# Optimization experiments

Measured on AMD Instinct MI355X. Metric: run time of the kernel, lower is better.

## Reference

```python
import jax, jax.numpy as jnp
import numpy as np

B, CH1, CH2, HID, T, E = 64, 3, 4, 16, 16384, 512

def setup_inputs() -> dict:
    key = jax.random.key(0)
    ks = jax.random.split(key, 12)
    s_t = 1.0 / np.sqrt(T)   # fan_in = input_dim for q/k/v projections
    s_e = 1.0 / np.sqrt(E)   # fan_in = embed_dim for out_proj
    return {
        "x":  jax.random.normal(ks[0], (B, 7, T), jnp.float32),
        "W1": jax.random.normal(ks[1], (HID, CH1), jnp.float32) / np.sqrt(CH1),
        "W2": jax.random.normal(ks[2], (HID, CH2), jnp.float32) / np.sqrt(CH2),
        "Wq": jax.random.normal(ks[3], (E, T), jnp.float32) * s_t,
        "bq": jnp.zeros((E,), jnp.float32),
        "Wk": jax.random.normal(ks[4], (E, T), jnp.float32) * s_t,
        "bk": jnp.zeros((E,), jnp.float32),
        "Wv": jax.random.normal(ks[5], (E, T), jnp.float32) * s_t,
        "bv": jnp.zeros((E,), jnp.float32),
        "Wo": jax.random.normal(ks[6], (T, E), jnp.float32) * s_e,
        "bo": jnp.zeros((T,), jnp.float32),
        "W3": jax.random.normal(ks[7], (CH1, HID), jnp.float32) / np.sqrt(HID),
    }

def reference(x, W1, W2, Wq, bq, Wk, bk, Wv, bv, Wo, bo, W3):
    p = x[:, :CH1]            # [B,3,T]  narrow(1,0,ch_1)
    c = x[:, 3:3 + CH2]       # [B,4,T]  narrow(1,3,ch_2)
    q = jnp.einsum('oc,bct->bot', W1, p)   # fc_1: [B,16,T]
    cc = jnp.einsum('oc,bct->bot', W2, c)  # fc_2: [B,16,T]
    # CrossAttention: Linears act on last dim (T -> E)
    Q = jnp.einsum('bct,et->bce', q, Wq) + bq    # [B,16,E]
    K = jnp.einsum('bct,et->bce', cc, Wk) + bk   # [B,16,E]
    V = jnp.einsum('bct,et->bce', cc, Wv) + bv   # [B,16,E]
    scale = 1.0 / np.sqrt(HID)                   # nch = 16 query channels
    attn_w = jax.nn.softmax(jnp.einsum('bce,bcf->bef', Q, K) * scale, axis=-1)  # [B,E,E]
    attn = jnp.einsum('bef,bcf->bce', attn_w, V)  # [B,16,E]
    out = jnp.einsum('bce,te->bct', attn, Wo) + bo  # out_proj: [B,16,T]
    y = jnp.einsum('oc,bct->bot', W3, out)          # fc_3: [B,3,T]
    return p + y
```

## Files before the change

kernel.cpp:

```cpp
#include <hip/hip_runtime.h>

#define BB 64
#define TT 16384
#define EE 512

typedef _Float16 half8 __attribute__((ext_vector_type(8)));
typedef float floatx4 __attribute__((ext_vector_type(4)));

static __device__ __forceinline__ half8 cvt_half8(float4 a, float4 b) {
  half8 h;
  h[0] = (_Float16)a.x; h[1] = (_Float16)a.y; h[2] = (_Float16)a.z; h[3] = (_Float16)a.w;
  h[4] = (_Float16)b.x; h[5] = (_Float16)b.y; h[6] = (_Float16)b.z; h[7] = (_Float16)b.w;
  return h;
}

static __device__ __forceinline__ void gload_lds16(const void* g, void* l) {
  __builtin_amdgcn_global_load_lds(
      (const __attribute__((address_space(1))) void*)g,
      (__attribute__((address_space(3))) void*)l, 16, 0, 0);
}

__global__ __launch_bounds__(256) void zero_ws(float4* __restrict__ p) {
  p[blockIdx.x * 256 + threadIdx.x] = (float4){0.f, 0.f, 0.f, 0.f};
}

__global__ __launch_bounds__(256) void proj_gemm(
    const float* __restrict__ x, const float* __restrict__ Wq,
    const float* __restrict__ Wk, const float* __restrict__ Wv,
    float* __restrict__ Xq, float* __restrict__ Xkv)
{
  __shared__ float Abuf[3][64 * 32];
  __shared__ float Bbuf[3][64 * 32];
  const int t = threadIdx.x;
  const int wave = t >> 6, lane = t & 63;
  const int quad = lane >> 4, l16 = lane & 15;
  const int wr = wave >> 1, wc = wave & 1;

  const int orig = blockIdx.x;
  const int logical = (orig & 7) * 352 + (orig >> 3);
  const int chunk = logical / 88;
  const int tile  = logical - chunk * 88;
  const int k0 = chunk << 9;

  int mtile, ntile, cpb, chan_base, ldout;
  const float* Wsrc;
  float* outC;
  if (tile < 24) {
    mtile = tile >> 3; ntile = tile & 7;
    cpb = 3; chan_base = 0; ldout = 512;
    Wsrc = Wq + (size_t)(ntile * 64) * TT;
    outC = Xq;
  } else {
    const int t2 = tile - 24;
    mtile = t2 >> 4; ntile = t2 & 15;
    cpb = 4; chan_base = 3; ldout = 1024;
    Wsrc = (ntile < 8) ? (Wk + (size_t)(ntile * 64) * TT)
                       : (Wv + (size_t)((ntile - 8) * 64) * TT);
    outC = Xkv;
  }

  const float* aSrc[2];
  const float* bSrc[2];
#pragma unroll
  for (int r = 0; r < 2; ++r) {
    const int i = (r * 4 + wave) * 64 + lane;
    const int row = i >> 3, u = i & 7;
    const int m = mtile * 64 + row;
    const int bidx = (cpb == 3) ? ((m * 21846) >> 16) : (m >> 2);
    const int j = m - bidx * cpb;
    const int swu = (u ^ (row & 7)) << 2;
    aSrc[r] = x + (size_t)(bidx * 7 + chan_base + j) * TT + k0 + swu;
    bSrc[r] = Wsrc + (size_t)row * TT + k0 + swu;
  }

  floatx4 acc[2][2];
#pragma unroll
  for (int rt = 0; rt < 2; ++rt)
#pragma unroll
    for (int ct = 0; ct < 2; ++ct)
      acc[rt][ct] = (floatx4){0.f, 0.f, 0.f, 0.f};

  const int sw = l16 & 7;

  auto stage = [&](int kt_, int buf_) {
    const int ko = kt_ * 32;
#pragma unroll
    for (int r = 0; r < 2; ++r) {
      gload_lds16(aSrc[r] + ko, &Abuf[buf_][(r * 4 + wave) * 256]);
      gload_lds16(bSrc[r] + ko, &Bbuf[buf_][(r * 4 + wave) * 256]);
    }
  };
  auto compute = [&](int buf_) {
    half8 hb[2], ha[2];
#pragma unroll
    for (int ct = 0; ct < 2; ++ct) {
      const int brow = wc * 32 + ct * 16 + l16;
      float4 b0 = *(const float4*)&Bbuf[buf_][brow * 32 + ((((quad << 1) | 0) ^ sw) << 2)];
      float4 b1 = *(const float4*)&Bbuf[buf_][brow * 32 + ((((quad << 1) | 1) ^ sw) << 2)];
      hb[ct] = cvt_half8(b0, b1);
    }
#pragma unroll
    for (int rt = 0; rt < 2; ++rt) {
      const int arow = wr * 32 + rt * 16 + l16;
      float4 a0 = *(const float4*)&Abuf[buf_][arow * 32 + ((((quad << 1) | 0) ^ sw) << 2)];
      float4 a1 = *(const float4*)&Abuf[buf_][arow * 32 + ((((quad << 1) | 1) ^ sw) << 2)];
      ha[rt] = cvt_half8(a0, a1);
    }
    __builtin_amdgcn_s_setprio(1);
#pragma unroll
    for (int rt = 0; rt < 2; ++rt)
#pragma unroll
      for (int ct = 0; ct < 2; ++ct)
        acc[rt][ct] = __builtin_amdgcn_mfma_f32_16x16x32_f16(ha[rt], hb[ct], acc[rt][ct], 0, 0, 0);
    __builtin_amdgcn_s_setprio(0);
  };

  stage(0, 0);
  stage(1, 1);
  asm volatile("s_waitcnt vmcnt(4)" ::: "memory");
  __builtin_amdgcn_s_barrier();
  __builtin_amdgcn_sched_barrier(0);

  int cur = 0;
#pragma unroll
  for (int kt = 0; kt < 14; ++kt) {
    const int nx2 = (cur + 2 >= 3) ? cur - 1 : cur + 2;
    stage(kt + 2, nx2);
    compute(cur);
    asm volatile("s_waitcnt vmcnt(4)" ::: "memory");
    __builtin_amdgcn_s_barrier();
    __builtin_amdgcn_sched_barrier(0);
    cur = (cur + 1 >= 3) ? 0 : cur + 1;
  }
  compute(cur);
  asm volatile("s_waitcnt vmcnt(0)" ::: "memory");
  __builtin_amdgcn_s_barrier();
  __builtin_amdgcn_sched_barrier(0);
  compute((cur + 1 >= 3) ? 0 : cur + 1);

#pragma unroll
  for (int rt = 0; rt < 2; ++rt) {
#pragma unroll
    for (int ct = 0; ct < 2; ++ct) {
      const int gr = mtile * 64 + wr * 32 + rt * 16 + quad * 4;
      const int gc = ntile * 64 + wc * 32 + ct * 16 + l16;
#pragma unroll
      for (int rg = 0; rg < 4; ++rg)
        atomicAdd(&outC[(size_t)(gr + rg) * ldout + gc], acc[rt][ct][rg]);
    }
  }
}

__global__ __launch_bounds__(256) void attn_mid(
    const float* __restrict__ Xq, const float* __restrict__ Xkv,
    const float* __restrict__ W1, const float* __restrict__ W2,
    const float* __restrict__ W3,
    const float* __restrict__ bq, const float* __restrict__ bk,
    const float* __restrict__ bv, _Float16* __restrict__ U)
{
  __shared__ float Ks[16][512];
  __shared__ float VW[3][512];
  __shared__ float Qs[16][64];
  __shared__ float Xs[4][512];
  __shared__ float W1s[48], W2s[64], W3s[48], W32s[12], w3sum[3];
  const int t = threadIdx.x;
  const int b = blockIdx.y;
  const int e0 = blockIdx.x * 64;

  if (t < 48) W1s[t] = W1[t];
  if (t >= 64 && t < 128) W2s[t - 64] = W2[t - 64];
  if (t >= 128 && t < 176) W3s[t - 128] = W3[t - 128];
  __syncthreads();
  if (t < 12) {
    const int o = t >> 2, jj = t & 3;
    float s = 0.f;
    for (int c = 0; c < 16; ++c) s += W3s[o * 16 + c] * W2s[c * 4 + jj];
    W32s[t] = s;
  }
  if (t >= 16 && t < 19) {
    const int o = t - 16;
    float s = 0.f;
    for (int c = 0; c < 16; ++c) s += W3s[o * 16 + c];
    w3sum[o] = s;
  }
  for (int i = t; i < 2048; i += 256) {
    const int jj = i >> 9, f = i & 511;
    Xs[jj][f] = Xkv[(size_t)(b * 4 + jj) * 1024 + f];
  }
  __syncthreads();
  for (int i = t; i < 8192; i += 256) {
    const int c = i >> 9, f = i & 511;
    float s = bk[f];
#pragma unroll
    for (int jj = 0; jj < 4; ++jj) s += W2s[c * 4 + jj] * Xs[jj][f];
    Ks[c][f] = s;
  }
  __syncthreads();
  for (int i = t; i < 2048; i += 256) {
    const int jj = i >> 9, f = i & 511;
    Xs[jj][f] = Xkv[(size_t)(b * 4 + jj) * 1024 + 512 + f];
  }
  __syncthreads();
  for (int i = t; i < 1536; i += 256) {
    const int o = i >> 9, f = i & 511;
    float s = w3sum[o] * bv[f];
#pragma unroll
    for (int jj = 0; jj < 4; ++jj) s += W32s[o * 4 + jj] * Xs[jj][f];
    VW[o][f] = s;
  }
  for (int i = t; i < 1024; i += 256) {
    const int c = i >> 6, el = i & 63;
    float s = bq[e0 + el];
#pragma unroll
    for (int jj = 0; jj < 3; ++jj)
      s += W1s[c * 3 + jj] * Xq[(size_t)(b * 3 + jj) * 512 + e0 + el];
    Qs[c][el] = s;
  }
  __syncthreads();

  const int wave = t >> 6, lane = t & 63;
  float vwr[3][8];
#pragma unroll
  for (int o = 0; o < 3; ++o) {
    float4 va = *(const float4*)&VW[o][lane * 8];
    float4 vb = *(const float4*)&VW[o][lane * 8 + 4];
    vwr[o][0] = va.x; vwr[o][1] = va.y; vwr[o][2] = va.z; vwr[o][3] = va.w;
    vwr[o][4] = vb.x; vwr[o][5] = vb.y; vwr[o][6] = vb.z; vwr[o][7] = vb.w;
  }

  for (int g = 0; g < 4; ++g) {
    const int el0 = wave * 16 + g * 4;
    float s[4][8];
#pragma unroll
    for (int e = 0; e < 4; ++e)
#pragma unroll
      for (int i = 0; i < 8; ++i) s[e][i] = 0.f;
#pragma unroll
    for (int c = 0; c < 16; ++c) {
      float4 k0 = *(const float4*)&Ks[c][lane * 8];
      float4 k1 = *(const float4*)&Ks[c][lane * 8 + 4];
      float4 qv = *(const float4*)&Qs[c][el0];
      float qa[4] = {qv.x, qv.y, qv.z, qv.w};
#pragma unroll
      for (int e = 0; e < 4; ++e) {
        const float q = qa[e];
        s[e][0] += q * k0.x; s[e][1] += q * k0.y; s[e][2] += q * k0.z; s[e][3] += q * k0.w;
        s[e][4] += q * k1.x; s[e][5] += q * k1.y; s[e][6] += q * k1.z; s[e][7] += q * k1.w;
      }
    }
#pragma unroll
    for (int e = 0; e < 4; ++e) {
      float mx = s[e][0];
#pragma unroll
      for (int i = 1; i < 8; ++i) mx = fmaxf(mx, s[e][i]);
#pragma unroll
      for (int off = 32; off; off >>= 1) mx = fmaxf(mx, __shfl_xor(mx, off));
      float p[8], sum = 0.f;
#pragma unroll
      for (int i = 0; i < 8; ++i) { p[i] = __expf(0.25f * (s[e][i] - mx)); sum += p[i]; }
      float u0 = 0.f, u1 = 0.f, u2 = 0.f;
#pragma unroll
      for (int i = 0; i < 8; ++i) {
        u0 += p[i] * vwr[0][i];
        u1 += p[i] * vwr[1][i];
        u2 += p[i] * vwr[2][i];
      }
#pragma unroll
      for (int off = 32; off; off >>= 1) {
        sum += __shfl_xor(sum, off);
        u0  += __shfl_xor(u0, off);
        u1  += __shfl_xor(u1, off);
        u2  += __shfl_xor(u2, off);
      }
      if (lane == 0) {
        const float inv = 1.0f / sum;
        const size_t base = (size_t)b * 3 * 512 + (e0 + el0 + e);
        U[base]        = (_Float16)(u0 * inv);
        U[base + 512]  = (_Float16)(u1 * inv);
        U[base + 1024] = (_Float16)(u2 * inv);
      }
    }
  }
}

__global__ __launch_bounds__(256) void out_gemm(
    const _Float16* __restrict__ U, const float* __restrict__ Wo,
    const float* __restrict__ x, const float* __restrict__ bo,
    const float* __restrict__ W3, float* __restrict__ outY)
{
  __shared__ _Float16 Au[3][64 * 32];
  __shared__ float    Bw[3][64 * 32];
  const int t = threadIdx.x;
  const int wave = t >> 6, lane = t & 63;
  const int quad = lane >> 4, l16 = lane & 15;
  const int mtile = blockIdx.y, ntile = blockIdx.x;

  float w3s[3];
#pragma unroll
  for (int o = 0; o < 3; ++o) {
    float s = 0.f;
#pragma unroll
    for (int c = 0; c < 16; ++c) s += W3[o * 16 + c];
    w3s[o] = s;
  }

  const int ai = wave * 64 + lane;
  const int arow_s = ai >> 2, au = ai & 3;
  const _Float16* aSrc = U + (size_t)(mtile * 64 + arow_s) * EE
                           + ((au ^ (arow_s & 3)) << 3);
  const float* bSrc[2];
#pragma unroll
  for (int r = 0; r < 2; ++r) {
    const int i = (r * 4 + wave) * 64 + lane;
    const int row = i >> 3, u = i & 7;
    bSrc[r] = Wo + (size_t)(ntile * 64 + row) * EE + ((u ^ (row & 7)) << 2);
  }

  floatx4 acc[4];
#pragma unroll
  for (int rt = 0; rt < 4; ++rt) acc[rt] = (floatx4){0.f, 0.f, 0.f, 0.f};

  const int brow = wave * 16 + l16;
  const int bsw = brow & 7;

  auto stage = [&](int kt_, int buf_) {
    gload_lds16(aSrc + kt_ * 32, &Au[buf_][wave * 512]);
#pragma unroll
    for (int r = 0; r < 2; ++r)
      gload_lds16(bSrc[r] + kt_ * 32, &Bw[buf_][(r * 4 + wave) * 256]);
  };
  auto compute = [&](int buf_) {
    float4 b0 = *(const float4*)&Bw[buf_][brow * 32 + ((((quad << 1) | 0) ^ bsw) << 2)];
    float4 b1 = *(const float4*)&Bw[buf_][brow * 32 + ((((quad << 1) | 1) ^ bsw) << 2)];
    const half8 hb = cvt_half8(b0, b1);
    half8 ha[4];
#pragma unroll
    for (int rt = 0; rt < 4; ++rt) {
      const int arow = rt * 16 + l16;
      ha[rt] = *(const half8*)&Au[buf_][arow * 32 + ((quad ^ (arow & 3)) << 3)];
    }
    __builtin_amdgcn_s_setprio(1);
#pragma unroll
    for (int rt = 0; rt < 4; ++rt)
      acc[rt] = __builtin_amdgcn_mfma_f32_16x16x32_f16(ha[rt], hb, acc[rt], 0, 0, 0);
    __builtin_amdgcn_s_setprio(0);
  };

  stage(0, 0);
  stage(1, 1);
  asm volatile("s_waitcnt vmcnt(3)" ::: "memory");
  __builtin_amdgcn_s_barrier();
  __builtin_amdgcn_sched_barrier(0);

  int cur = 0;
#pragma unroll
  for (int kt = 0; kt < 14; ++kt) {
    const int nx2 = (cur + 2 >= 3) ? cur - 1 : cur + 2;
    stage(kt + 2, nx2);
    compute(cur);
    asm volatile("s_waitcnt vmcnt(3)" ::: "memory");
    __builtin_amdgcn_s_barrier();
    __builtin_amdgcn_sched_barrier(0);
    cur = (cur + 1 >= 3) ? 0 : cur + 1;
  }
  compute(cur);
  asm volatile("s_waitcnt vmcnt(0)" ::: "memory");
  __builtin_amdgcn_s_barrier();
  __builtin_amdgcn_sched_barrier(0);
  compute((cur + 1 >= 3) ? 0 : cur + 1);

  const int tc = ntile * 64 + wave * 16 + l16;
  const float bot = bo[tc];
#pragma unroll
  for (int rt = 0; rt < 4; ++rt) {
    const int gr = mtile * 64 + rt * 16 + quad * 4;
#pragma unroll
    for (int rg = 0; rg < 4; ++rg) {
      const int rr = gr + rg;
      const int bb = rr / 3, oo = rr - bb * 3;
      const float v = acc[rt][rg]
                    + x[(size_t)(bb * 7 + oo) * TT + tc]
                    + w3s[oo] * bot;
      outY[(size_t)rr * TT + tc] = v;
    }
  }
}

extern "C" void kernel_launch(void* const* d_in, const int* in_sizes, int n_in,
                              void* d_out, int out_size, void* d_ws, size_t ws_size,
                              hipStream_t stream) {
  const float* x  = (const float*)d_in[0];
  const float* W1 = (const float*)d_in[1];
  const float* W2 = (const float*)d_in[2];
  const float* Wq = (const float*)d_in[3];
  const float* bq = (const float*)d_in[4];
  const float* Wk = (const float*)d_in[5];
  const float* bk = (const float*)d_in[6];
  const float* Wv = (const float*)d_in[7];
  const float* bv = (const float*)d_in[8];
  const float* Wo = (const float*)d_in[9];
  const float* bo = (const float*)d_in[10];
  const float* W3 = (const float*)d_in[11];
  float* out = (float*)d_out;

  char* ws = (char*)d_ws;
  float* Xq      = (float*)ws;
  float* Xkv     = (float*)(ws + 393216);
  _Float16* U    = (_Float16*)(ws + 1441792);

  zero_ws<<<dim3(352), 256, 0, stream>>>((float4*)ws);

  proj_gemm<<<dim3(2816), 256, 0, stream>>>(x, Wq, Wk, Wv, Xq, Xkv);
  attn_mid<<<dim3(8, BB), 256, 0, stream>>>(Xq, Xkv, W1, W2, W3, bq, bk, bv, U);
  out_gemm<<<dim3(256, 3), 256, 0, stream>>>(U, Wo, x, bo, W3, out);
}
```

Before: 277.0 us.

## Replace atomic split-K with partial buffers plus reduction, widen GEMM tiles

The projection GEMM drops atomicAdd accumulation and the zeroing kernel. Each K-chunk now writes plain stores into a per-chunk partial buffer, and a new reduce kernel sums the chunks into Xq and Xkv. The projection tile is widened to 128 columns and the split count is derived from workspace size (up to 16 chunks). The output GEMM K-step is doubled to 64. This trades atomic traffic and block count for a larger workspace, an extra reduction pass, and more shared memory per block, which may lower occupancy.

```diff
diff --git a/kernel.cpp b/kernel.cpp
--- a/kernel.cpp
+++ b/kernel.cpp
@@ -3,6 +3,9 @@
 #define BB 64
 #define TT 16384
 #define EE 512
+
+#define PSZ 360448
+#define PQ_OFF 98304
 
 typedef _Float16 half8 __attribute__((ext_vector_type(8)));
 typedef float floatx4 __attribute__((ext_vector_type(4)));
@@ -20,47 +23,44 @@
       (__attribute__((address_space(3))) void*)l, 16, 0, 0);
 }
 
-__global__ __launch_bounds__(256) void zero_ws(float4* __restrict__ p) {
-  p[blockIdx.x * 256 + threadIdx.x] = (float4){0.f, 0.f, 0.f, 0.f};
-}
-
 __global__ __launch_bounds__(256) void proj_gemm(
     const float* __restrict__ x, const float* __restrict__ Wq,
     const float* __restrict__ Wk, const float* __restrict__ Wv,
-    float* __restrict__ Xq, float* __restrict__ Xkv)
+    float* __restrict__ P, int KL, int NT, int cpx)
 {
   __shared__ float Abuf[3][64 * 32];
-  __shared__ float Bbuf[3][64 * 32];
+  __shared__ float Bbuf[3][128 * 32];
   const int t = threadIdx.x;
   const int wave = t >> 6, lane = t & 63;
   const int quad = lane >> 4, l16 = lane & 15;
   const int wr = wave >> 1, wc = wave & 1;
 
   const int orig = blockIdx.x;
-  const int logical = (orig & 7) * 352 + (orig >> 3);
-  const int chunk = logical / 88;
-  const int tile  = logical - chunk * 88;
-  const int k0 = chunk << 9;
-
-  int mtile, ntile, cpb, chan_base, ldout;
+  const int logical = (orig & 7) * cpx + (orig >> 3);
+  const int chunk = logical / 44;
+  const int tile  = logical - chunk * 44;
+  const int k0 = chunk * KL;
+
+  int mtile, ntile, cpb, chan_base;
   const float* Wsrc;
-  float* outC;
-  if (tile < 24) {
-    mtile = tile >> 3; ntile = tile & 7;
-    cpb = 3; chan_base = 0; ldout = 512;
-    Wsrc = Wq + (size_t)(ntile * 64) * TT;
-    outC = Xq;
+  int pbase;
+  if (tile < 12) {
+    mtile = tile >> 2; ntile = tile & 3;
+    cpb = 3; chan_base = 0;
+    Wsrc = Wq + (size_t)(ntile * 128) * TT;
+    pbase = 0;
   } else {
-    const int t2 = tile - 24;
-    mtile = t2 >> 4; ntile = t2 & 15;
-    cpb = 4; chan_base = 3; ldout = 1024;
-    Wsrc = (ntile < 8) ? (Wk + (size_t)(ntile * 64) * TT)
-                       : (Wv + (size_t)((ntile - 8) * 64) * TT);
-    outC = Xkv;
-  }
+    const int t2 = tile - 12;
+    mtile = t2 >> 3; ntile = t2 & 7;
+    cpb = 4; chan_base = 3;
+    Wsrc = (ntile < 4) ? (Wk + (size_t)(ntile * 128) * TT)
+                       : (Wv + (size_t)((ntile - 4) * 128) * TT);
+    pbase = PQ_OFF;
+  }
+  const int ldout = (tile < 12) ? 512 : 1024;
 
   const float* aSrc[2];
-  const float* bSrc[2];
+  const float* bSrc[4];
 #pragma unroll
   for (int r = 0; r < 2; ++r) {
     const int i = (r * 4 + wave) * 64 + lane;
@@ -68,33 +68,38 @@
     const int m = mtile * 64 + row;
     const int bidx = (cpb == 3) ? ((m * 21846) >> 16) : (m >> 2);
     const int j = m - bidx * cpb;
-    const int swu = (u ^ (row & 7)) << 2;
-    aSrc[r] = x + (size_t)(bidx * 7 + chan_base + j) * TT + k0 + swu;
-    bSrc[r] = Wsrc + (size_t)row * TT + k0 + swu;
-  }
-
-  floatx4 acc[2][2];
+    aSrc[r] = x + (size_t)(bidx * 7 + chan_base + j) * TT + k0
+                + ((u ^ (row & 7)) << 2);
+  }
+#pragma unroll
+  for (int r = 0; r < 4; ++r) {
+    const int i = (r * 4 + wave) * 64 + lane;
+    const int row = i >> 3, u = i & 7;
+    bSrc[r] = Wsrc + (size_t)row * TT + k0 + ((u ^ (row & 7)) << 2);
+  }
+
+  floatx4 acc[2][4];
 #pragma unroll
   for (int rt = 0; rt < 2; ++rt)
 #pragma unroll
-    for (int ct = 0; ct < 2; ++ct)
+    for (int ct = 0; ct < 4; ++ct)
       acc[rt][ct] = (floatx4){0.f, 0.f, 0.f, 0.f};
-
-  const int sw = l16 & 7;
 
   auto stage = [&](int kt_, int buf_) {
     const int ko = kt_ * 32;
 #pragma unroll
-    for (int r = 0; r < 2; ++r) {
+    for (int r = 0; r < 2; ++r)
       gload_lds16(aSrc[r] + ko, &Abuf[buf_][(r * 4 + wave) * 256]);
+#pragma unroll
+    for (int r = 0; r < 4; ++r)
       gload_lds16(bSrc[r] + ko, &Bbuf[buf_][(r * 4 + wave) * 256]);
-    }
   };
   auto compute = [&](int buf_) {
-    half8 hb[2], ha[2];
-#pragma unroll
-    for (int ct = 0; ct < 2; ++ct) {
-      const int brow = wc * 32 + ct * 16 + l16;
+    half8 hb[4], ha[2];
+#pragma unroll
+    for (int ct = 0; ct < 4; ++ct) {
+      const int brow = wc * 64 + ct * 16 + l16;
+      const int sw = brow & 7;
       float4 b0 = *(const float4*)&Bbuf[buf_][brow * 32 + ((((quad << 1) | 0) ^ sw) << 2)];
       float4 b1 = *(const float4*)&Bbuf[buf_][brow * 32 + ((((quad << 1) | 1) ^ sw) << 2)];
       hb[ct] = cvt_half8(b0, b1);
@@ -102,6 +107,7 @@
 #pragma unroll
     for (int rt = 0; rt < 2; ++rt) {
       const int arow = wr * 32 + rt * 16 + l16;
+      const int sw = arow & 7;
       float4 a0 = *(const float4*)&Abuf[buf_][arow * 32 + ((((quad << 1) | 0) ^ sw) << 2)];
       float4 a1 = *(const float4*)&Abuf[buf_][arow * 32 + ((((quad << 1) | 1) ^ sw) << 2)];
       ha[rt] = cvt_half8(a0, a1);
@@ -110,24 +116,23 @@
 #pragma unroll
     for (int rt = 0; rt < 2; ++rt)
 #pragma unroll
-      for (int ct = 0; ct < 2; ++ct)
+      for (int ct = 0; ct < 4; ++ct)
         acc[rt][ct] = __builtin_amdgcn_mfma_f32_16x16x32_f16(ha[rt], hb[ct], acc[rt][ct], 0, 0, 0);
     __builtin_amdgcn_s_setprio(0);
   };
 
   stage(0, 0);
   stage(1, 1);
-  asm volatile("s_waitcnt vmcnt(4)" ::: "memory");
+  asm volatile("s_waitcnt vmcnt(6)" ::: "memory");
   __builtin_amdgcn_s_barrier();
   __builtin_amdgcn_sched_barrier(0);
 
   int cur = 0;
-#pragma unroll
-  for (int kt = 0; kt < 14; ++kt) {
+  for (int kt = 0; kt < NT - 2; ++kt) {
     const int nx2 = (cur + 2 >= 3) ? cur - 1 : cur + 2;
     stage(kt + 2, nx2);
     compute(cur);
-    asm volatile("s_waitcnt vmcnt(4)" ::: "memory");
+    asm volatile("s_waitcnt vmcnt(6)" ::: "memory");
     __builtin_amdgcn_s_barrier();
     __builtin_amdgcn_sched_barrier(0);
     cur = (cur + 1 >= 3) ? 0 : cur + 1;
@@ -138,17 +143,29 @@
   __builtin_amdgcn_sched_barrier(0);
   compute((cur + 1 >= 3) ? 0 : cur + 1);
 
+  float* outP = P + (size_t)chunk * PSZ + pbase;
 #pragma unroll
   for (int rt = 0; rt < 2; ++rt) {
 #pragma unroll
-    for (int ct = 0; ct < 2; ++ct) {
+    for (int ct = 0; ct < 4; ++ct) {
       const int gr = mtile * 64 + wr * 32 + rt * 16 + quad * 4;
-      const int gc = ntile * 64 + wc * 32 + ct * 16 + l16;
+      const int gc = ntile * 128 + wc * 64 + ct * 16 + l16;
 #pragma unroll
       for (int rg = 0; rg < 4; ++rg)
-        atomicAdd(&outC[(size_t)(gr + rg) * ldout + gc], acc[rt][ct][rg]);
-    }
-  }
+        outP[(size_t)(gr + rg) * ldout + gc] = acc[rt][ct][rg];
+    }
+  }
+}
+
+__global__ __launch_bounds__(256) void reduce_p(
+    const floatx4* __restrict__ P4, float* __restrict__ Xq,
+    float* __restrict__ Xkv, int CH)
+{
+  const int i = blockIdx.x * 256 + threadIdx.x;
+  floatx4 s = P4[i];
+  for (int c = 1; c < CH; ++c) s += P4[(size_t)c * (PSZ / 4) + i];
+  if (i < PQ_OFF / 4) ((floatx4*)Xq)[i] = s;
+  else                ((floatx4*)Xkv)[i - PQ_OFF / 4] = s;
 }
 
 __global__ __launch_bounds__(256) void attn_mid(
@@ -288,8 +305,8 @@
     const float* __restrict__ x, const float* __restrict__ bo,
     const float* __restrict__ W3, float* __restrict__ outY)
 {
-  __shared__ _Float16 Au[3][64 * 32];
-  __shared__ float    Bw[3][64 * 32];
+  __shared__ _Float16 Au[3][64 * 64];
+  __shared__ float    Bw[3][64 * 64];
   const int t = threadIdx.x;
   const int wave = t >> 6, lane = t & 63;
   const int quad = lane >> 4, l16 = lane & 15;
@@ -304,15 +321,18 @@
     w3s[o] = s;
   }
 
-  const int ai = wave * 64 + lane;
-  const int arow_s = ai >> 2, au = ai & 3;
-  const _Float16* aSrc = U + (size_t)(mtile * 64 + arow_s) * EE
-                           + ((au ^ (arow_s & 3)) << 3);
-  const float* bSrc[2];
+  const _Float16* aSrc[2];
 #pragma unroll
   for (int r = 0; r < 2; ++r) {
     const int i = (r * 4 + wave) * 64 + lane;
     const int row = i >> 3, u = i & 7;
+    aSrc[r] = U + (size_t)(mtile * 64 + row) * EE + ((u ^ (row & 7)) << 3);
+  }
+  const float* bSrc[4];
+#pragma unroll
+  for (int r = 0; r < 4; ++r) {
+    const int i = (r * 4 + wave) * 64 + lane;
+    const int row = i >> 4, u = i & 15;
     bSrc[r] = Wo + (size_t)(ntile * 64 + row) * EE + ((u ^ (row & 7)) << 2);
   }
 
@@ -324,41 +344,47 @@
   const int bsw = brow & 7;
 
   auto stage = [&](int kt_, int buf_) {
-    gload_lds16(aSrc + kt_ * 32, &Au[buf_][wave * 512]);
+    const int ko = kt_ * 64;
 #pragma unroll
     for (int r = 0; r < 2; ++r)
-      gload_lds16(bSrc[r] + kt_ * 32, &Bw[buf_][(r * 4 + wave) * 256]);
+      gload_lds16(aSrc[r] + ko, &Au[buf_][(r * 4 + wave) * 512]);
+#pragma unroll
+    for (int r = 0; r < 4; ++r)
+      gload_lds16(bSrc[r] + ko, &Bw[buf_][(r * 4 + wave) * 256]);
   };
   auto compute = [&](int buf_) {
-    float4 b0 = *(const float4*)&Bw[buf_][brow * 32 + ((((quad << 1) | 0) ^ bsw) << 2)];
-    float4 b1 = *(const float4*)&Bw[buf_][brow * 32 + ((((quad << 1) | 1) ^ bsw) << 2)];
-    const half8 hb = cvt_half8(b0, b1);
-    half8 ha[4];
-#pragma unroll
-    for (int rt = 0; rt < 4; ++rt) {
-      const int arow = rt * 16 + l16;
-      ha[rt] = *(const half8*)&Au[buf_][arow * 32 + ((quad ^ (arow & 3)) << 3)];
-    }
-    __builtin_amdgcn_s_setprio(1);
-#pragma unroll
-    for (int rt = 0; rt < 4; ++rt)
-      acc[rt] = __builtin_amdgcn_mfma_f32_16x16x32_f16(ha[rt], hb, acc[rt], 0, 0, 0);
-    __builtin_amdgcn_s_setprio(0);
+#pragma unroll
+    for (int kk = 0; kk < 2; ++kk) {
+      float4 b0 = *(const float4*)&Bw[buf_][brow * 64 + (((kk * 8 + quad * 2 + 0) ^ bsw) << 2)];
+      float4 b1 = *(const float4*)&Bw[buf_][brow * 64 + (((kk * 8 + quad * 2 + 1) ^ bsw) << 2)];
+      const half8 hb = cvt_half8(b0, b1);
+      half8 ha[4];
+#pragma unroll
+      for (int rt = 0; rt < 4; ++rt) {
+        const int arow = rt * 16 + l16;
+        ha[rt] = *(const half8*)&Au[buf_][arow * 64 + (((kk * 4 + quad) ^ (arow & 7)) << 3)];
+      }
+      __builtin_amdgcn_s_setprio(1);
+#pragma unroll
+      for (int rt = 0; rt < 4; ++rt)
+        acc[rt] = __builtin_amdgcn_mfma_f32_16x16x32_f16(ha[rt], hb, acc[rt], 0, 0, 0);
+      __builtin_amdgcn_s_setprio(0);
+    }
   };
 
   stage(0, 0);
   stage(1, 1);
-  asm volatile("s_waitcnt vmcnt(3)" ::: "memory");
+  asm volatile("s_waitcnt vmcnt(6)" ::: "memory");
   __builtin_amdgcn_s_barrier();
   __builtin_amdgcn_sched_barrier(0);
 
   int cur = 0;
 #pragma unroll
-  for (int kt = 0; kt < 14; ++kt) {
+  for (int kt = 0; kt < 6; ++kt) {
     const int nx2 = (cur + 2 >= 3) ? cur - 1 : cur + 2;
     stage(kt + 2, nx2);
     compute(cur);
-    asm volatile("s_waitcnt vmcnt(3)" ::: "memory");
+    asm volatile("s_waitcnt vmcnt(6)" ::: "memory");
     __builtin_amdgcn_s_barrier();
     __builtin_amdgcn_sched_barrier(0);
     cur = (cur + 1 >= 3) ? 0 : cur + 1;
@@ -407,10 +433,17 @@
   float* Xq      = (float*)ws;
   float* Xkv     = (float*)(ws + 393216);
   _Float16* U    = (_Float16*)(ws + 1441792);
-
-  zero_ws<<<dim3(352), 256, 0, stream>>>((float4*)ws);
-
-  proj_gemm<<<dim3(2816), 256, 0, stream>>>(x, Wq, Wk, Wv, Xq, Xkv);
+  float* P       = (float*)(ws + 1638400);
+
+  int CH = 16;
+  while (CH > 2 && ws_size < 1638400ull + (size_t)CH * PSZ * 4) CH >>= 1;
+  const int KL = 16384 / CH;
+  const int NT = KL / 32;
+  const int nblk = 44 * CH;
+  const int cpx = nblk / 8;
+
+  proj_gemm<<<dim3(nblk), 256, 0, stream>>>(x, Wq, Wk, Wv, P, KL, NT, cpx);
+  reduce_p<<<dim3(352), 256, 0, stream>>>((const floatx4*)P, Xq, Xkv, CH);
   attn_mid<<<dim3(8, BB), 256, 0, stream>>>(Xq, Xkv, W1, W2, W3, bq, bk, bv, U);
   out_gemm<<<dim3(256, 3), 256, 0, stream>>>(U, Wo, x, bo, W3, out);
 }
```

Result: slower. 287.0 us (+3.6%).
